# Performance work log

Hardware: AMD Instinct MI355X
Metric: run time of the kernel (lower is better)

Reference implementation:

```python
import jax, jax.numpy as jnp
import numpy as np

A0 = 0.529177249
SIGMA = jnp.array([0.5515909, 1.8886297, 1.3225029, 1.2316629, 2.1884933, 1.7750372, 1.3677907, 1.3820058], dtype=jnp.float32)

N_MOL, N_ATOM, AEV_LEN = 256, 384, 384
DIMS = [160, 128, 96]


def _mlp(x, W1, b1, W2, b2, W3, b3, W4, b4):
    celu = lambda v: jax.nn.celu(v, alpha=0.1)
    h = celu(x @ W1.T + b1)
    h = celu(h @ W2.T + b2)
    h = celu(h @ W3.T + b3)
    return jax.nn.softplus(h @ W4.T + b4)  # (Nn, 1)


def setup_inputs() -> dict:
    key = jax.random.key(0)
    ks = jax.random.split(key, 12)
    species = jax.random.randint(ks[0], (N_MOL, N_ATOM), 0, 8)
    # pad the tail of each molecule (species == -1)
    species = species.at[:, N_ATOM - 64:].set(-1)
    coordinates = jax.random.normal(ks[1], (N_MOL, N_ATOM, 3), dtype=jnp.float32) * 3.0
    net_charge = jax.random.normal(ks[2], (N_MOL,), dtype=jnp.float32)
    aev = jax.random.normal(ks[3], (N_MOL, N_ATOM, AEV_LEN), dtype=jnp.float32)
    in_dim = AEV_LEN + 2
    d1, d2, d3 = DIMS
    s = 0.05
    W1 = jax.random.normal(ks[4], (d1, in_dim), dtype=jnp.float32) * s
    b1 = jnp.zeros((d1,), dtype=jnp.float32)
    W2 = jax.random.normal(ks[5], (d2, d1), dtype=jnp.float32) * s
    b2 = jnp.zeros((d2,), dtype=jnp.float32)
    W3 = jax.random.normal(ks[6], (d3, d2), dtype=jnp.float32) * s
    b3 = jnp.zeros((d3,), dtype=jnp.float32)
    W4 = jax.random.normal(ks[7], (1, d3), dtype=jnp.float32) * s
    b4 = jnp.zeros((1,), dtype=jnp.float32)
    return {"species": species, "coordinates": coordinates, "net_charge": net_charge,
            "aev": aev, "W1": W1, "b1": b1, "W2": W2, "b2": b2,
            "W3": W3, "b3": b3, "W4": W4, "b4": b4}


def reference(species, coordinates, net_charge, aev, W1, b1, W2, b2, W3, b3, W4, b4):
    N, n = species.shape
    # pairwise distances in atomic units (eps avoids div-by-zero on diagonal)
    diff = coordinates[:, None, :, :] - coordinates[:, :, None, :]  # (N,n,n,3)
    distances = jnp.sqrt(jnp.sum(diff * diff, axis=-1) + 1e-16) / A0  # (N,n,n)

    padding_mask = (species != -1).astype(coordinates.dtype)  # (N,n)
    pair_mask = padding_mask[:, :, None] * padding_mask[:, None, :]  # (N,n,n)
    num_atoms = padding_mask.sum(axis=1)  # (N,)

    # ESP kernel j_ij (constant across iterations)
    sig = SIGMA[species]  # negative padding index wraps to last sigma, as in torch
    sig_sqsum = jnp.maximum(sig[:, None, :] ** 2 + sig[:, :, None] ** 2, 1e-8)
    j_ij = jax.lax.erf(distances / jnp.sqrt(2.0 * sig_sqsum)) / distances  # (N,n,n)
    diag_mask = 1.0 - jnp.eye(n, dtype=coordinates.dtype)
    j_masked = j_ij * pair_mask * diag_mask[None]  # fuse masks once

    mask_flat = species.reshape(-1) != -1  # (N*n,)
    aev_flat = aev.reshape(N * n, -1)
    pred_charges = jnp.zeros((N * n,), dtype=coordinates.dtype)
    esp = jnp.zeros((N * n,), dtype=coordinates.dtype)

    for _ in range(4):
        feats = jnp.concatenate(
            [aev_flat, pred_charges[:, None], esp[:, None]], axis=1)  # (Nn, aev+2)
        chi_all = _mlp(feats, W1, b1, W2, b2, W3, b3, W4, b4)[:, 0]
        chi = jnp.where(mask_flat, chi_all, 0.0)  # padded atoms keep 0 (masked_scatter)
        chi_copy = chi.reshape(N, n)
        chi_sum = chi_copy.sum(axis=-1)  # (N,)
        k_net = 1.0 + jnp.abs(net_charge) / chi_sum
        chi_mean = chi_sum / num_atoms
        k_p = jnp.where(net_charge > 0, k_net, 1.0)
        k_n = jnp.where(net_charge < 0, k_net, 1.0)
        iter_charges = (-k_n[:, None] * chi_copy + (k_p * chi_mean)[:, None]) * padding_mask
        # esp_j = sum_i q_i * j_ij[i, j] (masked)
        esp2d = jnp.sum(iter_charges[:, :, None] * j_masked, axis=1)  # (N,n)
        pred_charges = iter_charges.reshape(-1)
        esp = esp2d.reshape(-1)

    return species, pred_charges.reshape(N, n)
```

## Files before the change

kernel.cpp:

```cpp
#include <hip/hip_runtime.h>
#include <math.h>

#define NMOL 256
#define NATOM 384
#define NN (NMOL*NATOM)
#define A0C  0.529177249f
#define A0_INV (1.0f/0.529177249f)

typedef short bf16x8 __attribute__((ext_vector_type(8)));
typedef float f32x4  __attribute__((ext_vector_type(4)));
typedef _Float16 h16x8 __attribute__((ext_vector_type(8)));

__constant__ float c_sigma[8] = {0.5515909f, 1.8886297f, 1.3225029f, 1.2316629f,
                                 2.1884933f, 1.7750372f, 1.3677907f, 1.3820058f};

__device__ __forceinline__ short f2b(float f) {
    unsigned u = __float_as_uint(f);
    u = (u + 0x7fffu + ((u >> 16) & 1u)) >> 16;
    return (short)u;
}
__device__ __forceinline__ float b2f(short s) {
    return __uint_as_float(((unsigned)(unsigned short)s) << 16);
}
__device__ __forceinline__ float celu01(float v) {
    return v > 0.f ? v : 0.1f * expm1f(10.f * v);
}
__device__ __forceinline__ bf16x8 cvt8(f32x4 a, f32x4 b) {
    bf16x8 r;
    r[0] = f2b(a.x); r[1] = f2b(a.y); r[2] = f2b(a.z); r[3] = f2b(a.w);
    r[4] = f2b(b.x); r[5] = f2b(b.y); r[6] = f2b(b.z); r[7] = f2b(b.w);
    return r;
}

__device__ __forceinline__ float erf_fast(float x) {
    float t = __builtin_amdgcn_rcpf(fmaf(0.3275911f, x, 1.0f));
    float p = fmaf(t, 1.061405429f, -1.453152027f);
    p = fmaf(t, p, 1.421413741f);
    p = fmaf(t, p, -0.284496736f);
    p = fmaf(t, p, 0.254829592f);
    p = p * t;
    float e = __builtin_amdgcn_exp2f(-x * x * 1.4426950408889634f);
    return fmaf(-p, e, 1.0f);
}

template<int N, int K>
__global__ __launch_bounds__(256, 4)
void gemm0_k(const float* __restrict__ A, const short* __restrict__ Bw,
             const float* __restrict__ bias, short* __restrict__ Cout)
{
    constexpr int NK = K / 32;
    constexpr int NF = N / 32;
    constexpr int N2 = N / 2;
    constexpr int AROW = 40, BROW = 40;
    constexpr int ASZ = 64 * AROW;
    constexpr int BSZ = N * BROW;
    constexpr int AB  = 2 * ASZ + 2 * BSZ;
    constexpr int CSZ = 64 * N;
    constexpr int SM  = AB > CSZ ? AB : CSZ;
    constexpr int NB  = (N * 4 + 255) / 256;

    __shared__ short smem[SM];
    short* As0 = smem;
    short* As1 = smem + ASZ;
    short* Bs0 = smem + 2 * ASZ;
    short* Bs1 = smem + 2 * ASZ + BSZ;
    short* Cs  = smem;

    const int t    = threadIdx.x;
    const int lane = t & 63;
    const int wave = t >> 6;
    const int wm   = wave >> 1, wn = wave & 1;
    const int l15  = lane & 15, l4 = lane >> 4;
    const int m0   = blockIdx.x * 64;
    const int arow = t >> 2, aseg = t & 3;
    const float* a_f32 = A + ((size_t)m0 + arow) * K + aseg * 8;

    f32x4 af0, af1;
    bf16x8 br[NB];

    auto loadA = [&](int k0) {
        af0 = *(const f32x4*)(a_f32 + k0);
        af1 = *(const f32x4*)(a_f32 + k0 + 4);
    };
    auto loadB = [&](int k0) {
        #pragma unroll
        for (int ci = 0; ci < NB; ++ci) {
            int c = ci * 256 + t;
            if ((N * 4) % 256 == 0 || c < N * 4) {
                int row = c >> 2, half = c & 3;
                br[ci] = *(const bf16x8*)(Bw + (size_t)row * K + k0 + half * 8);
            }
        }
    };
    auto writeA = [&](short* dst) {
        *(bf16x8*)&dst[arow * AROW + aseg * 8] = cvt8(af0, af1);
    };
    auto writeB = [&](short* dst) {
        #pragma unroll
        for (int ci = 0; ci < NB; ++ci) {
            int c = ci * 256 + t;
            if ((N * 4) % 256 == 0 || c < N * 4) {
                int row = c >> 2, half = c & 3;
                *(bf16x8*)&dst[row * BROW + half * 8] = br[ci];
            }
        }
    };

    f32x4 acc[2][NF] = {};

    loadA(0); loadB(0);
    writeA(As0); writeB(Bs0);
    __syncthreads();

    int cur = 0;
    for (int ks = 0; ks < NK; ++ks) {
        if (ks + 1 < NK) { loadA((ks + 1) * 32); loadB((ks + 1) * 32); }
        short* Ac = cur ? As1 : As0;
        short* Bc = cur ? Bs1 : Bs0;
        bf16x8 a[2];
        #pragma unroll
        for (int mf = 0; mf < 2; ++mf)
            a[mf] = *(const bf16x8*)&Ac[(wm * 32 + mf * 16 + l15) * AROW + l4 * 8];
        #pragma unroll
        for (int nf = 0; nf < NF; ++nf) {
            bf16x8 b = *(const bf16x8*)&Bc[(wn * N2 + nf * 16 + l15) * BROW + l4 * 8];
            #pragma unroll
            for (int mf = 0; mf < 2; ++mf)
                acc[mf][nf] = __builtin_amdgcn_mfma_f32_16x16x32_bf16(a[mf], b, acc[mf][nf], 0, 0, 0);
        }
        if (ks + 1 < NK) {
            writeA(cur ? As0 : As1);
            writeB(cur ? Bs0 : Bs1);
            __syncthreads();
            cur ^= 1;
        }
    }
    __syncthreads();

    #pragma unroll
    for (int nf = 0; nf < NF; ++nf) {
        int col = wn * N2 + nf * 16 + l15;
        float bc = bias[col];
        #pragma unroll
        for (int mf = 0; mf < 2; ++mf)
            #pragma unroll
            for (int r = 0; r < 4; ++r)
                Cs[(wm * 32 + mf * 16 + l4 * 4 + r) * N + col] = f2b(acc[mf][nf][r] + bc);
    }
    __syncthreads();
    #pragma unroll
    for (int i = 0; i < NF; ++i) {
        int c = i * 256 + t;
        *(bf16x8*)(Cout + (size_t)m0 * N + c * 8) = *(const bf16x8*)&Cs[c * 8];
    }
}

__global__ __launch_bounds__(256, 3)
void mlp23_kernel(const short* __restrict__ h1p, const short* __restrict__ W2b,
                  const float* __restrict__ b2, const short* __restrict__ W3b,
                  const float* __restrict__ b3, const float* __restrict__ W4,
                  const float* __restrict__ b4,
                  const float* __restrict__ qv, const float* __restrict__ espv,
                  const float* __restrict__ w1qp, const float* __restrict__ w1ep,
                  const int* __restrict__ species, float* __restrict__ chi)
{
    constexpr int K1 = 160, N1 = 128, K2 = 128, N3 = 96;
    constexpr int AROW = 40, BROW = 40, H2ROW = 136;

    __shared__ short As[2][64 * AROW];
    __shared__ short Bs[2][N1 * BROW];
    __shared__ short H2[64 * H2ROW];
    __shared__ float wq_s[K1], we_s[K1], w4_s[N3], b3_s[N3];
    __shared__ float chp[2][64];

    const int t    = threadIdx.x;
    const int lane = t & 63;
    const int wave = t >> 6;
    const int wm   = wave >> 1, wn = wave & 1;
    const int l15  = lane & 15, l4 = lane >> 4;
    const int m0   = blockIdx.x * 64;
    const int arow = t >> 2, aseg = t & 3;
    const size_t agrow = (size_t)m0 + arow;

    if (t < K1) { wq_s[t] = w1qp[t]; we_s[t] = w1ep[t]; }
    if (t < N3) { w4_s[t] = W4[t]; b3_s[t] = b3[t]; }

    const short* a_b16 = h1p + agrow * K1 + aseg * 8;
    const float qr = qv[agrow];
    const float er = espv[agrow] + espv[NN + agrow] + espv[2 * (size_t)NN + agrow]
                   + espv[3 * (size_t)NN + agrow];

    bf16x8 ah;
    bf16x8 br[2];

    auto loadA = [&](int k0) { ah = *(const bf16x8*)(a_b16 + k0); };
    auto loadB1 = [&](int k0) {
        #pragma unroll
        for (int ci = 0; ci < 2; ++ci) {
            int c = ci * 256 + t;
            int row = c >> 2, half = c & 3;
            br[ci] = *(const bf16x8*)(W2b + (size_t)row * K1 + k0 + half * 8);
        }
    };
    auto writeA = [&](short* dst, int k0) {
        bf16x8 o;
        #pragma unroll
        for (int j = 0; j < 8; ++j) {
            float v = b2f(ah[j]) + qr * wq_s[k0 + aseg * 8 + j]
                                 + er * we_s[k0 + aseg * 8 + j];
            o[j] = f2b(celu01(v));
        }
        *(bf16x8*)&dst[arow * AROW + aseg * 8] = o;
    };
    auto writeB1 = [&](short* dst) {
        #pragma unroll
        for (int ci = 0; ci < 2; ++ci) {
            int c = ci * 256 + t;
            int row = c >> 2, half = c & 3;
            *(bf16x8*)&dst[row * BROW + half * 8] = br[ci];
        }
    };

    f32x4 acc[2][4] = {};
    loadA(0); loadB1(0);
    __syncthreads();
    writeA(As[0], 0); writeB1(Bs[0]);
    __syncthreads();

    int cur = 0;
    for (int ks = 0; ks < 5; ++ks) {
        if (ks + 1 < 5) { loadA((ks + 1) * 32); loadB1((ks + 1) * 32); }
        const short* Ac = As[cur];
        const short* Bc = Bs[cur];
        bf16x8 a[2];
        #pragma unroll
        for (int mf = 0; mf < 2; ++mf)
            a[mf] = *(const bf16x8*)&Ac[(wm * 32 + mf * 16 + l15) * AROW + l4 * 8];
        #pragma unroll
        for (int nf = 0; nf < 4; ++nf) {
            bf16x8 b = *(const bf16x8*)&Bc[(wn * 64 + nf * 16 + l15) * BROW + l4 * 8];
            #pragma unroll
            for (int mf = 0; mf < 2; ++mf)
                acc[mf][nf] = __builtin_amdgcn_mfma_f32_16x16x32_bf16(a[mf], b, acc[mf][nf], 0, 0, 0);
        }
        if (ks + 1 < 5) {
            writeA(As[cur ^ 1], (ks + 1) * 32);
            writeB1(Bs[cur ^ 1]);
            __syncthreads();
            cur ^= 1;
        }
    }

    #pragma unroll
    for (int nf = 0; nf < 4; ++nf) {
        int col = wn * 64 + nf * 16 + l15;
        float bc = b2[col];
        #pragma unroll
        for (int mf = 0; mf < 2; ++mf)
            #pragma unroll
            for (int r = 0; r < 4; ++r)
                H2[(wm * 32 + mf * 16 + l4 * 4 + r) * H2ROW + col] =
                    f2b(celu01(acc[mf][nf][r] + bc));
    }

    auto loadB2 = [&](int k0) {
        #pragma unroll
        for (int ci = 0; ci < 2; ++ci) {
            int c = ci * 256 + t;
            if (c < N3 * 4) {
                int row = c >> 2, half = c & 3;
                br[ci] = *(const bf16x8*)(W3b + (size_t)row * K2 + k0 + half * 8);
            }
        }
    };
    auto writeB2 = [&](short* dst) {
        #pragma unroll
        for (int ci = 0; ci < 2; ++ci) {
            int c = ci * 256 + t;
            if (c < N3 * 4) {
                int row = c >> 2, half = c & 3;
                *(bf16x8*)&dst[row * BROW + half * 8] = br[ci];
            }
        }
    };

    loadB2(0);
    __syncthreads();
    writeB2(Bs[0]);
    __syncthreads();

    f32x4 acc2[2][3] = {};
    cur = 0;
    for (int ks = 0; ks < 4; ++ks) {
        if (ks + 1 < 4) loadB2((ks + 1) * 32);
        const short* Bc = Bs[cur];
        bf16x8 a[2];
        #pragma unroll
        for (int mf = 0; mf < 2; ++mf)
            a[mf] = *(const bf16x8*)&H2[(wm * 32 + mf * 16 + l15) * H2ROW + ks * 32 + l4 * 8];
        #pragma unroll
        for (int nf = 0; nf < 3; ++nf) {
            bf16x8 b = *(const bf16x8*)&Bc[(wn * 48 + nf * 16 + l15) * BROW + l4 * 8];
            #pragma unroll
            for (int mf = 0; mf < 2; ++mf)
                acc2[mf][nf] = __builtin_amdgcn_mfma_f32_16x16x32_bf16(a[mf], b, acc2[mf][nf], 0, 0, 0);
        }
        if (ks + 1 < 4) {
            writeB2(Bs[cur ^ 1]);
            __syncthreads();
            cur ^= 1;
        }
    }

    float val[2][4];
    #pragma unroll
    for (int mf = 0; mf < 2; ++mf)
        #pragma unroll
        for (int r = 0; r < 4; ++r) val[mf][r] = 0.f;
    #pragma unroll
    for (int nf = 0; nf < 3; ++nf) {
        int col = wn * 48 + nf * 16 + l15;
        float bc = b3_s[col];
        float wc = w4_s[col];
        #pragma unroll
        for (int mf = 0; mf < 2; ++mf)
            #pragma unroll
            for (int r = 0; r < 4; ++r)
                val[mf][r] += celu01(acc2[mf][nf][r] + bc) * wc;
    }
    #pragma unroll
    for (int off = 1; off < 16; off <<= 1)
        #pragma unroll
        for (int mf = 0; mf < 2; ++mf)
            #pragma unroll
            for (int r = 0; r < 4; ++r)
                val[mf][r] += __shfl_xor(val[mf][r], off, 64);
    if (l15 == 0) {
        #pragma unroll
        for (int mf = 0; mf < 2; ++mf)
            #pragma unroll
            for (int r = 0; r < 4; ++r)
                chp[wn][wm * 32 + mf * 16 + l4 * 4 + r] = val[mf][r];
    }
    __syncthreads();
    if (t < 64) {
        float s = chp[0][t] + chp[1][t] + b4[0];
        s = fmaxf(s, 0.f) + log1pf(expf(-fabsf(s)));
        chi[m0 + t] = (species[m0 + t] != -1) ? s : 0.f;
    }
}

__global__ __launch_bounds__(384)
void jbuild_kernel(const float* __restrict__ coords, const int* __restrict__ species,
                   _Float16* __restrict__ J)
{
    __shared__ float cx[NATOM], cy[NATOM], cz[NATOM], s2[NATOM], mk[NATOM];
    int m = blockIdx.x, it0 = blockIdx.y * 48;
    int j = threadIdx.x;
    int idx = m * NATOM + j;
    float rx = coords[(size_t)idx * 3 + 0];
    float ry = coords[(size_t)idx * 3 + 1];
    float rz = coords[(size_t)idx * 3 + 2];
    int sp = species[idx];
    float sig = c_sigma[sp < 0 ? 7 : sp];
    cx[j] = rx; cy[j] = ry; cz[j] = rz;
    s2[j] = sig * sig;
    float maskj = (sp != -1) ? 1.f : 0.f;
    mk[j] = maskj;
    __syncthreads();
    float s2j = s2[j];
    #pragma unroll 4
    for (int ii = 0; ii < 48; ++ii) {
        int i = it0 + ii;
        float dx = cx[i] - rx, dy = cy[i] - ry, dz = cz[i] - rz;
        float d2 = fmaf(dx, dx, fmaf(dy, dy, dz * dz)) + 1e-16f;
        float rs = __builtin_amdgcn_rsqf(d2);
        float d  = d2 * rs * A0_INV;
        float ss = fmaxf(s2[i] + s2j, 1e-8f);
        float x  = d * __builtin_amdgcn_rsqf(2.f * ss);
        float val = erf_fast(x) * rs * A0C;
        val *= maskj * mk[i];
        val = (i == j) ? 0.f : val;
        J[((size_t)m * NATOM + i) * NATOM + j] = (_Float16)val;
    }
}

template<bool DO_MV>
__global__ __launch_bounds__(384)
void espmv_kernel(const float* __restrict__ chi, const int* __restrict__ species,
                  const float* __restrict__ netq, const _Float16* __restrict__ J,
                  float* __restrict__ q, float* __restrict__ esp_part)
{
    __shared__ float red[512], redc[512];
    __shared__ float qs[DO_MV ? 96 : 1];
    __shared__ float part[DO_MV ? 8 : 1][DO_MV ? 384 : 1];
    int m = blockIdx.x, ic = blockIdx.y;
    int t = threadIdx.x;
    int idx = m * NATOM + t;
    float c = chi[idx];
    int sp = species[idx];
    float mask = (sp != -1) ? 1.f : 0.f;
    red[t] = c; redc[t] = mask;
    if (t < 128) { red[NATOM + t] = 0.f; redc[NATOM + t] = 0.f; }
    __syncthreads();
    for (int s = 256; s > 0; s >>= 1) {
        if (t < s) { red[t] += red[t + s]; redc[t] += redc[t + s]; }
        __syncthreads();
    }
    float chi_sum = red[0], na = redc[0];
    float Q = netq[m];
    float k_net = 1.f + fabsf(Q) / chi_sum;
    float chi_mean = chi_sum / na;
    float k_p = (Q > 0.f) ? k_net : 1.f;
    float k_n = (Q < 0.f) ? k_net : 1.f;
    float qj = (-k_n * c + k_p * chi_mean) * mask;
    if (ic == 0) q[idx] = qj;

    if (DO_MV) {
        if (t >= ic * 96 && t < ic * 96 + 96) qs[t - ic * 96] = qj;
        __syncthreads();
        int jv = t % 48, isub = t / 48;
        int j0 = jv * 8;
        float acc[8] = {};
        #pragma unroll 4
        for (int k = 0; k < 12; ++k) {
            int il = isub * 12 + k;
            int i = ic * 96 + il;
            h16x8 h = *(const h16x8*)&J[((size_t)m * NATOM + i) * NATOM + j0];
            float qi = qs[il];
            #pragma unroll
            for (int r = 0; r < 8; ++r) acc[r] = fmaf(qi, (float)h[r], acc[r]);
        }
        #pragma unroll
        for (int r = 0; r < 8; ++r) part[isub][j0 + r] = acc[r];
        __syncthreads();
        float s = 0.f;
        #pragma unroll
        for (int g = 0; g < 8; ++g) s += part[g][t];
        esp_part[(size_t)ic * NN + idx] = s;
    }
}

template<bool DO_ESP>
__global__ __launch_bounds__(384)
void espq_kernel(const float* __restrict__ chi, const int* __restrict__ species,
                 const float* __restrict__ netq, const float* __restrict__ coords,
                 float* __restrict__ q, float* __restrict__ esp)
{
    __shared__ float red[512], redc[512];
    __shared__ float cx[NATOM], cy[NATOM], cz[NATOM], s2[NATOM], qs[NATOM];
    int m = blockIdx.x, j = threadIdx.x;
    int idx = m * NATOM + j;
    float c = chi[idx];
    int sp = species[idx];
    float mask = (sp != -1) ? 1.f : 0.f;
    red[j] = c; redc[j] = mask;
    if (j < 128) { red[NATOM + j] = 0.f; redc[NATOM + j] = 0.f; }
    __syncthreads();
    for (int s = 256; s > 0; s >>= 1) {
        if (j < s) { red[j] += red[j + s]; redc[j] += redc[j + s]; }
        __syncthreads();
    }
    float chi_sum = red[0], na = redc[0];
    float Q = netq[m];
    float k_net = 1.f + fabsf(Q) / chi_sum;
    float chi_mean = chi_sum / na;
    float k_p = (Q > 0.f) ? k_net : 1.f;
    float k_n = (Q < 0.f) ? k_net : 1.f;
    float qj = (-k_n * c + k_p * chi_mean) * mask;
    q[idx] = qj;

    if (DO_ESP) {
        float rx = coords[(size_t)idx * 3 + 0];
        float ry = coords[(size_t)idx * 3 + 1];
        float rz = coords[(size_t)idx * 3 + 2];
        cx[j] = rx; cy[j] = ry; cz[j] = rz;
        float sig = c_sigma[sp < 0 ? 7 : sp];
        s2[j] = sig * sig;
        qs[j] = qj;
        __syncthreads();
        float s2j = s2[j];
        float acc = 0.f;
        for (int i = 0; i < NATOM; ++i) {
            float dx = cx[i] - rx, dy = cy[i] - ry, dz = cz[i] - rz;
            float d2 = fmaf(dx, dx, fmaf(dy, dy, dz * dz)) + 1e-16f;
            float rs = __builtin_amdgcn_rsqf(d2);
            float d  = d2 * rs * A0_INV;
            float ss = fmaxf(s2[i] + s2j, 1e-8f);
            float x  = d * __builtin_amdgcn_rsqf(2.f * ss);
            float val = erf_fast(x) * rs * A0C;
            acc += (i == j) ? 0.f : qs[i] * val;
        }
        esp[idx] = (mask != 0.f) ? acc : 0.f;
    }
}

__global__ __launch_bounds__(256)
void wcvt_kernel(const float* __restrict__ W1, const float* __restrict__ W2,
                 const float* __restrict__ W3,
                 short* __restrict__ W1b, short* __restrict__ W2b,
                 short* __restrict__ W3b, float* __restrict__ w1q,
                 float* __restrict__ w1e)
{
    int i = blockIdx.x * 256 + threadIdx.x;
    if (i < 160 * 384) {
        int r = i / 384, cc = i % 384;
        W1b[i] = f2b(W1[(size_t)r * 386 + cc]);
    }
    int j = i - 160 * 384;
    if (j >= 0 && j < 128 * 160) W2b[j] = f2b(W2[j]);
    int k2 = j - 128 * 160;
    if (k2 >= 0 && k2 < 96 * 128) W3b[k2] = f2b(W3[k2]);
    if (i < 160) {
        w1q[i] = W1[(size_t)i * 386 + 384];
        w1e[i] = W1[(size_t)i * 386 + 385];
    }
}

__global__ __launch_bounds__(256)
void out_kernel(const int* __restrict__ species, const float* __restrict__ q,
                float* __restrict__ out)
{
    int i = blockIdx.x * 256 + threadIdx.x;
    out[i] = (float)species[i];
    out[NN + i] = q[i];
}

extern "C" void kernel_launch(void* const* d_in, const int* in_sizes, int n_in,
                              void* d_out, int out_size, void* d_ws, size_t ws_size,
                              hipStream_t stream)
{
    const int*   species = (const int*)  d_in[0];
    const float* coords  = (const float*)d_in[1];
    const float* netq    = (const float*)d_in[2];
    const float* aev     = (const float*)d_in[3];
    const float* W1 = (const float*)d_in[4];
    const float* b1 = (const float*)d_in[5];
    const float* W2 = (const float*)d_in[6];
    const float* b2 = (const float*)d_in[7];
    const float* W3 = (const float*)d_in[8];
    const float* b3 = (const float*)d_in[9];
    const float* W4 = (const float*)d_in[10];
    const float* b4 = (const float*)d_in[11];

    float* q    = (float*)d_ws;
    float* chi  = q + NN;
    float* espp = chi + NN;
    float* w1q  = espp + 4 * (size_t)NN;
    float* w1e  = w1q + 160;
    short* W1b  = (short*)(w1e + 160);
    short* W2b  = W1b + 160 * 384;
    short* W3b  = W2b + 128 * 160;
    short* h1p  = W3b + 96 * 128;
    _Float16* J = (_Float16*)(h1p + (size_t)NN * 160);

    const size_t NEED = (size_t)((char*)(J + (size_t)NN * 384) - (char*)d_ws);
    const bool use_J = (ws_size >= NEED);

    hipMemsetAsync(d_ws, 0, 6 * (size_t)NN * sizeof(float), stream);
    wcvt_kernel<<<(160 * 384 + 128 * 160 + 96 * 128 + 255) / 256, 256, 0, stream>>>(
        W1, W2, W3, W1b, W2b, W3b, w1q, w1e);

    if (use_J)
        jbuild_kernel<<<dim3(NMOL, 8), 384, 0, stream>>>(coords, species, J);

    gemm0_k<160, 384><<<NN / 64, 256, 0, stream>>>(aev, W1b, b1, h1p);

    for (int it = 0; it < 4; ++it) {
        mlp23_kernel<<<NN / 64, 256, 0, stream>>>(
            h1p, W2b, b2, W3b, b3, W4, b4, q, espp, w1q, w1e, species, chi);
        if (use_J) {
            if (it < 3)
                espmv_kernel<true><<<dim3(NMOL, 4), 384, 0, stream>>>(
                    chi, species, netq, J, q, espp);
            else
                espmv_kernel<false><<<dim3(NMOL, 1), 384, 0, stream>>>(
                    chi, species, netq, J, q, espp);
        } else {
            if (it < 3)
                espq_kernel<true><<<NMOL, 384, 0, stream>>>(
                    chi, species, netq, coords, q, espp);
            else
                espq_kernel<false><<<NMOL, 384, 0, stream>>>(
                    chi, species, netq, coords, q, espp);
        }
    }

    out_kernel<<<NN / 256, 256, 0, stream>>>(species, q, (float*)d_out);
}
```

Baseline: 304.6 us.

## Load MLP operands directly from global memory, use fast CELU and wave-shuffle reductions

```diff
diff --git a/kernel.cpp b/kernel.cpp
--- a/kernel.cpp
+++ b/kernel.cpp
@@ -23,7 +23,8 @@
     return __uint_as_float(((unsigned)(unsigned short)s) << 16);
 }
 __device__ __forceinline__ float celu01(float v) {
-    return v > 0.f ? v : 0.1f * expm1f(10.f * v);
+    float e = __builtin_amdgcn_exp2f(v * 14.426950408889634f);
+    return v > 0.f ? v : fmaf(0.1f, e, -0.1f);
 }
 __device__ __forceinline__ bf16x8 cvt8(f32x4 a, f32x4 b) {
     bf16x8 r;
@@ -155,7 +156,7 @@
     }
 }
 
-__global__ __launch_bounds__(256, 3)
+__global__ __launch_bounds__(256, 4)
 void mlp23_kernel(const short* __restrict__ h1p, const short* __restrict__ W2b,
                   const float* __restrict__ b2, const short* __restrict__ W3b,
                   const float* __restrict__ b3, const float* __restrict__ W4,
@@ -164,11 +165,9 @@
                   const float* __restrict__ w1qp, const float* __restrict__ w1ep,
                   const int* __restrict__ species, float* __restrict__ chi)
 {
-    constexpr int K1 = 160, N1 = 128, K2 = 128, N3 = 96;
-    constexpr int AROW = 40, BROW = 40, H2ROW = 136;
-
-    __shared__ short As[2][64 * AROW];
-    __shared__ short Bs[2][N1 * BROW];
+    constexpr int K1 = 160, K2 = 128, N3 = 96;
+    constexpr int H2ROW = 140;
+
     __shared__ short H2[64 * H2ROW];
     __shared__ float wq_s[K1], we_s[K1], w4_s[N3], b3_s[N3];
     __shared__ float chp[2][64];
@@ -179,75 +178,47 @@
     const int wm   = wave >> 1, wn = wave & 1;
     const int l15  = lane & 15, l4 = lane >> 4;
     const int m0   = blockIdx.x * 64;
-    const int arow = t >> 2, aseg = t & 3;
-    const size_t agrow = (size_t)m0 + arow;
 
     if (t < K1) { wq_s[t] = w1qp[t]; we_s[t] = w1ep[t]; }
     if (t < N3) { w4_s[t] = W4[t]; b3_s[t] = b3[t]; }
 
-    const short* a_b16 = h1p + agrow * K1 + aseg * 8;
-    const float qr = qv[agrow];
-    const float er = espv[agrow] + espv[NN + agrow] + espv[2 * (size_t)NN + agrow]
-                   + espv[3 * (size_t)NN + agrow];
-
-    bf16x8 ah;
-    bf16x8 br[2];
-
-    auto loadA = [&](int k0) { ah = *(const bf16x8*)(a_b16 + k0); };
-    auto loadB1 = [&](int k0) {
-        #pragma unroll
-        for (int ci = 0; ci < 2; ++ci) {
-            int c = ci * 256 + t;
-            int row = c >> 2, half = c & 3;
-            br[ci] = *(const bf16x8*)(W2b + (size_t)row * K1 + k0 + half * 8);
-        }
-    };
-    auto writeA = [&](short* dst, int k0) {
-        bf16x8 o;
-        #pragma unroll
-        for (int j = 0; j < 8; ++j) {
-            float v = b2f(ah[j]) + qr * wq_s[k0 + aseg * 8 + j]
-                                 + er * we_s[k0 + aseg * 8 + j];
-            o[j] = f2b(celu01(v));
-        }
-        *(bf16x8*)&dst[arow * AROW + aseg * 8] = o;
-    };
-    auto writeB1 = [&](short* dst) {
-        #pragma unroll
-        for (int ci = 0; ci < 2; ++ci) {
-            int c = ci * 256 + t;
-            int row = c >> 2, half = c & 3;
-            *(bf16x8*)&dst[row * BROW + half * 8] = br[ci];
-        }
-    };
+    int rowg[2];
+    float qrow[2], erow[2];
+    #pragma unroll
+    for (int mf = 0; mf < 2; ++mf) {
+        rowg[mf] = m0 + wm * 32 + mf * 16 + l15;
+        qrow[mf] = qv[rowg[mf]];
+        erow[mf] = espv[rowg[mf]] + espv[NN + rowg[mf]]
+                 + espv[2 * (size_t)NN + rowg[mf]] + espv[3 * (size_t)NN + rowg[mf]];
+    }
+    __syncthreads();
 
     f32x4 acc[2][4] = {};
-    loadA(0); loadB1(0);
-    __syncthreads();
-    writeA(As[0], 0); writeB1(Bs[0]);
-    __syncthreads();
-
-    int cur = 0;
+    #pragma unroll
     for (int ks = 0; ks < 5; ++ks) {
-        if (ks + 1 < 5) { loadA((ks + 1) * 32); loadB1((ks + 1) * 32); }
-        const short* Ac = As[cur];
-        const short* Bc = Bs[cur];
+        const int k0 = ks * 32 + l4 * 8;
+        f32x4 wq0 = *(const f32x4*)&wq_s[k0];
+        f32x4 wq1 = *(const f32x4*)&wq_s[k0 + 4];
+        f32x4 we0 = *(const f32x4*)&we_s[k0];
+        f32x4 we1 = *(const f32x4*)&we_s[k0 + 4];
         bf16x8 a[2];
         #pragma unroll
-        for (int mf = 0; mf < 2; ++mf)
-            a[mf] = *(const bf16x8*)&Ac[(wm * 32 + mf * 16 + l15) * AROW + l4 * 8];
+        for (int mf = 0; mf < 2; ++mf) {
+            bf16x8 h = *(const bf16x8*)(h1p + (size_t)rowg[mf] * K1 + k0);
+            #pragma unroll
+            for (int j = 0; j < 4; ++j) {
+                float v = b2f(h[j]) + qrow[mf] * wq0[j] + erow[mf] * we0[j];
+                a[mf][j] = f2b(celu01(v));
+                float v2 = b2f(h[j + 4]) + qrow[mf] * wq1[j] + erow[mf] * we1[j];
+                a[mf][j + 4] = f2b(celu01(v2));
+            }
+        }
         #pragma unroll
         for (int nf = 0; nf < 4; ++nf) {
-            bf16x8 b = *(const bf16x8*)&Bc[(wn * 64 + nf * 16 + l15) * BROW + l4 * 8];
+            bf16x8 b = *(const bf16x8*)(W2b + (size_t)(wn * 64 + nf * 16 + l15) * K1 + k0);
             #pragma unroll
             for (int mf = 0; mf < 2; ++mf)
                 acc[mf][nf] = __builtin_amdgcn_mfma_f32_16x16x32_bf16(a[mf], b, acc[mf][nf], 0, 0, 0);
-        }
-        if (ks + 1 < 5) {
-            writeA(As[cur ^ 1], (ks + 1) * 32);
-            writeB1(Bs[cur ^ 1]);
-            __syncthreads();
-            cur ^= 1;
         }
     }
 
@@ -262,53 +233,21 @@
                 H2[(wm * 32 + mf * 16 + l4 * 4 + r) * H2ROW + col] =
                     f2b(celu01(acc[mf][nf][r] + bc));
     }
-
-    auto loadB2 = [&](int k0) {
-        #pragma unroll
-        for (int ci = 0; ci < 2; ++ci) {
-            int c = ci * 256 + t;
-            if (c < N3 * 4) {
-                int row = c >> 2, half = c & 3;
-                br[ci] = *(const bf16x8*)(W3b + (size_t)row * K2 + k0 + half * 8);
-            }
-        }
-    };
-    auto writeB2 = [&](short* dst) {
-        #pragma unroll
-        for (int ci = 0; ci < 2; ++ci) {
-            int c = ci * 256 + t;
-            if (c < N3 * 4) {
-                int row = c >> 2, half = c & 3;
-                *(bf16x8*)&dst[row * BROW + half * 8] = br[ci];
-            }
-        }
-    };
-
-    loadB2(0);
-    __syncthreads();
-    writeB2(Bs[0]);
     __syncthreads();
 
     f32x4 acc2[2][3] = {};
-    cur = 0;
+    #pragma unroll
     for (int ks = 0; ks < 4; ++ks) {
-        if (ks + 1 < 4) loadB2((ks + 1) * 32);
-        const short* Bc = Bs[cur];
         bf16x8 a[2];
         #pragma unroll
         for (int mf = 0; mf < 2; ++mf)
             a[mf] = *(const bf16x8*)&H2[(wm * 32 + mf * 16 + l15) * H2ROW + ks * 32 + l4 * 8];
         #pragma unroll
         for (int nf = 0; nf < 3; ++nf) {
-            bf16x8 b = *(const bf16x8*)&Bc[(wn * 48 + nf * 16 + l15) * BROW + l4 * 8];
+            bf16x8 b = *(const bf16x8*)(W3b + (size_t)(wn * 48 + nf * 16 + l15) * K2 + ks * 32 + l4 * 8);
             #pragma unroll
             for (int mf = 0; mf < 2; ++mf)
                 acc2[mf][nf] = __builtin_amdgcn_mfma_f32_16x16x32_bf16(a[mf], b, acc2[mf][nf], 0, 0, 0);
-        }
-        if (ks + 1 < 4) {
-            writeB2(Bs[cur ^ 1]);
-            __syncthreads();
-            cur ^= 1;
         }
     }
 
@@ -391,23 +330,26 @@
                   const float* __restrict__ netq, const _Float16* __restrict__ J,
                   float* __restrict__ q, float* __restrict__ esp_part)
 {
-    __shared__ float red[512], redc[512];
+    __shared__ float pw[6], pwc[6];
     __shared__ float qs[DO_MV ? 96 : 1];
     __shared__ float part[DO_MV ? 8 : 1][DO_MV ? 384 : 1];
     int m = blockIdx.x, ic = blockIdx.y;
     int t = threadIdx.x;
+    int lane = t & 63, wv = t >> 6;
     int idx = m * NATOM + t;
     float c = chi[idx];
     int sp = species[idx];
     float mask = (sp != -1) ? 1.f : 0.f;
-    red[t] = c; redc[t] = mask;
-    if (t < 128) { red[NATOM + t] = 0.f; redc[NATOM + t] = 0.f; }
-    __syncthreads();
-    for (int s = 256; s > 0; s >>= 1) {
-        if (t < s) { red[t] += red[t + s]; redc[t] += redc[t + s]; }
-        __syncthreads();
-    }
-    float chi_sum = red[0], na = redc[0];
+    float sc = c, sm = mask;
+    #pragma unroll
+    for (int off = 1; off < 64; off <<= 1) {
+        sc += __shfl_xor(sc, off, 64);
+        sm += __shfl_xor(sm, off, 64);
+    }
+    if (lane == 0) { pw[wv] = sc; pwc[wv] = sm; }
+    __syncthreads();
+    float chi_sum = pw[0] + pw[1] + pw[2] + pw[3] + pw[4] + pw[5];
+    float na      = pwc[0] + pwc[1] + pwc[2] + pwc[3] + pwc[4] + pwc[5];
     float Q = netq[m];
     float k_net = 1.f + fabsf(Q) / chi_sum;
     float chi_mean = chi_sum / na;
```

Measured after the change: 257.4 us. 15.5% less time.
